# Optimization experiments

Measured on AMD Instinct MI355X. Metric: run time of the kernel, lower is better.

Reference implementation:

```python
import jax, jax.numpy as jnp
import numpy as np

B, SQ, SKV, D, H = 2, 2048, 2048, 1024, 16
HD = D // H

def setup_inputs() -> dict:
    key = jax.random.key(0)
    ks = jax.random.split(key, 11)
    def xavier(k, shape):
        fan_in, fan_out = shape[1], shape[0]
        lim = jnp.sqrt(6.0 / (fan_in + fan_out))
        return jax.random.uniform(k, shape, jnp.float32, -lim, lim)
    return {
        'query': jax.random.normal(ks[0], (B, SQ, D), jnp.float32),
        'key': jax.random.normal(ks[1], (B, SKV, D), jnp.float32),
        'value': jax.random.normal(ks[2], (B, SKV, D), jnp.float32),
        'Wq': xavier(ks[3], (D, D)), 'bq': jnp.zeros((D,), jnp.float32),
        'Wk': xavier(ks[4], (D, D)), 'bk': jnp.zeros((D,), jnp.float32),
        'Wv': xavier(ks[5], (D, D)), 'bv': jnp.zeros((D,), jnp.float32),
        'Wo': xavier(ks[6], (D, D)), 'bo': jnp.zeros((D,), jnp.float32),
    }

def reference(query, key, value, Wq, bq, Wk, bk, Wv, bv, Wo, bo):
    # Linear uses y = x @ W.T + b (torch convention, W: [out, in])
    Q = query @ Wq.T + bq   # [B, SQ, D]
    K = key @ Wk.T + bk     # [B, SKV, D]
    V = value @ Wv.T + bv   # [B, SKV, D]
    Q = Q.reshape(B, SQ, H, HD).transpose(0, 2, 1, 3)   # [B,H,SQ,HD]
    K = K.reshape(B, SKV, H, HD).transpose(0, 2, 1, 3)  # [B,H,SKV,HD]
    V = V.reshape(B, SKV, H, HD).transpose(0, 2, 1, 3)
    scores = jnp.einsum('bhqd,bhkd->bhqk', Q, K) / jnp.sqrt(jnp.float32(HD))
    probs = jax.nn.softmax(scores, axis=-1)  # dropout is identity at eval
    ctx = jnp.einsum('bhqk,bhkd->bhqd', probs, V)
    ctx = ctx.transpose(0, 2, 1, 3).reshape(B, SQ, D)
    return ctx @ Wo.T + bo
```

## Files before the change

### kernel.cpp

```cpp
#include <hip/hip_runtime.h>

#define DIM   1024
#define NHEAD 16
#define HDIM  64
#define BATCH 2
#define SEQ   2048
#define MTOT  4096

typedef unsigned short u16;
typedef unsigned int   u32;
typedef __attribute__((ext_vector_type(8))) short bf16x8;
typedef __attribute__((ext_vector_type(4))) float f32x4;
typedef __attribute__((ext_vector_type(4))) u32   u32x4;

#define QSCALE 0.18033688011112042f
#define EXP2F(x) __builtin_amdgcn_exp2f(x)
#define SWAP32(a, b) asm volatile("v_permlane32_swap_b32 %0, %1" : "+v"(a), "+v"(b))
#define SWAP16(a, b) asm volatile("v_permlane16_swap_b32 %0, %1" : "+v"(a), "+v"(b))

__device__ __forceinline__ void gload_lds16(const void* g, void* l) {
  __builtin_amdgcn_global_load_lds((const __attribute__((address_space(1))) void*)g,
                                   (__attribute__((address_space(3))) void*)l, 16, 0, 0);
}

__device__ __forceinline__ u16 f32_to_bf16(float f) {
  union { float f; u32 u; } v; v.f = f;
  u32 r = v.u + 0x7fffu + ((v.u >> 16) & 1u);
  return (u16)(r >> 16);
}

__device__ __forceinline__ u32 pack_bf16(float a, float b) {
  return (u32)f32_to_bf16(a) | ((u32)f32_to_bf16(b) << 16);
}

struct CvtArgs {
  const float* s[7];
  u16*         d[7];
  int          n8[7];
};

__global__ __launch_bounds__(256) void cvt_all(CvtArgs a) {
  const int z = blockIdx.z;
  const float* s = a.s[z];
  u16* d = a.d[z];
  const int n8 = a.n8[z];
  const int stride = gridDim.x * blockDim.x;
  for (int i = blockIdx.x * blockDim.x + threadIdx.x; i < n8; i += stride) {
    float4 x = ((const float4*)s)[2 * i], y = ((const float4*)s)[2 * i + 1];
    u32x4 o;
    o[0] = pack_bf16(x.x, x.y); o[1] = pack_bf16(x.z, x.w);
    o[2] = pack_bf16(y.x, y.y); o[3] = pack_bf16(y.z, y.w);
    *(u32x4*)&d[(size_t)i * 8] = o;
  }
}

template<int MF, bool OUTF32, bool BIAS_ROW>
__device__ __forceinline__ void gemm_body(
    const u16* __restrict__ X, const u16* __restrict__ W,
    const float* __restrict__ bias, void* __restrict__ Cv, int ldc, float scale,
    int m0, int n0)
{
  __shared__ __align__(16) u16 ldsA[32 * 4 * 64];
  __shared__ __align__(16) u16 ldsB[128 * 64];
  const int tid  = threadIdx.x;
  const int lane = tid & 63;
  const int wid  = tid >> 6;
  const int wr   = wid >> 1, wc = wid & 1;
  const int srow = tid >> 3;
  const int scs  = tid & 7;

  f32x4 acc[MF][4];
#pragma unroll
  for (int mf = 0; mf < MF; ++mf)
#pragma unroll
    for (int nf = 0; nf < 4; ++nf)
#pragma unroll
      for (int r = 0; r < 4; ++r) acc[mf][nf][r] = 0.f;

  for (int kt = 0; kt < DIM; kt += 64) {
    __syncthreads();
#pragma unroll
    for (int call = 0; call < MF; ++call) {
      int row = call * 32 + srow;
      int lc  = scs ^ (row & 7);
      gload_lds16(X + (size_t)(m0 + row) * DIM + kt + lc * 8,
                  &ldsA[(row * 8 + scs) * 8]);
    }
#pragma unroll
    for (int call = 0; call < 4; ++call) {
      int row = call * 32 + srow;
      int lc  = scs ^ (row & 7);
      gload_lds16(W + (size_t)(n0 + row) * DIM + kt + lc * 8,
                  &ldsB[(row * 8 + scs) * 8]);
    }
    __syncthreads();
#pragma unroll
    for (int ks = 0; ks < 2; ++ks) {
      bf16x8 af[MF], bfr[4];
#pragma unroll
      for (int mf = 0; mf < MF; ++mf) {
        int row = wr * (16 * MF) + mf * 16 + (lane & 15);
        int ch  = (ks * 4 + (lane >> 4)) ^ (row & 7);
        af[mf] = *(const bf16x8*)&ldsA[row * 64 + ch * 8];
      }
#pragma unroll
      for (int nf = 0; nf < 4; ++nf) {
        int row = wc * 64 + nf * 16 + (lane & 15);
        int ch  = (ks * 4 + (lane >> 4)) ^ (row & 7);
        bfr[nf] = *(const bf16x8*)&ldsB[row * 64 + ch * 8];
      }
#pragma unroll
      for (int mf = 0; mf < MF; ++mf)
#pragma unroll
        for (int nf = 0; nf < 4; ++nf)
          acc[mf][nf] = __builtin_amdgcn_mfma_f32_16x16x32_bf16(
              af[mf], bfr[nf], acc[mf][nf], 0, 0, 0);
    }
  }
#pragma unroll
  for (int nf = 0; nf < 4; ++nf) {
    int col = n0 + wc * 64 + nf * 16 + (lane & 15);
    float bcol = BIAS_ROW ? 0.f : bias[col];
#pragma unroll
    for (int mf = 0; mf < MF; ++mf) {
      int rbase = m0 + wr * (16 * MF) + mf * 16 + ((lane >> 4) << 2);
#pragma unroll
      for (int r = 0; r < 4; ++r) {
        float bv = BIAS_ROW ? bias[rbase + r] : bcol;
        float v = (acc[mf][nf][r] + bv) * scale;
        if (OUTF32) ((float*)Cv)[(size_t)(rbase + r) * ldc + col] = v;
        else        ((u16*)Cv)[(size_t)(rbase + r) * ldc + col] = f32_to_bf16(v);
      }
    }
  }
}

__global__ __launch_bounds__(256, 2) void gemm_proj_kernel(
    const u16* __restrict__ q, const u16* __restrict__ k, const u16* __restrict__ v,
    const u16* __restrict__ wq, const u16* __restrict__ wk, const u16* __restrict__ wv,
    const float* __restrict__ bq, const float* __restrict__ bk, const float* __restrict__ bv,
    u16* __restrict__ oq, u16* __restrict__ ok, u16* __restrict__ ovt)
{
  const int bid = blockIdx.x;
  const int wk_ = (bid & 7) * 96 + (bid >> 3);
  const int z = wk_ >> 8, rem = wk_ & 255;
  const int ty = rem >> 3, tx = rem & 7;
  if (z == 0)
    gemm_body<4, false, false>(q, wq, bq, oq, DIM, QSCALE, ty * 128, tx * 128);
  else if (z == 1)
    gemm_body<4, false, false>(k, wk, bk, ok, DIM, 1.0f, ty * 128, tx * 128);
  else
    gemm_body<4, false, true>(wv, v, bv, ovt, MTOT, 1.0f, tx * 128, ty * 128);
}

__global__ __launch_bounds__(256, 2) void gemm_o_kernel(
    const u16* __restrict__ x, const u16* __restrict__ w,
    const float* __restrict__ b, float* __restrict__ c)
{
  const int bid = blockIdx.x;
  const int wk_ = (bid & 7) * 64 + (bid >> 3);
  const int ty = wk_ >> 3, tx = wk_ & 7;
  gemm_body<2, true, false>(x, w, b, c, DIM, 1.0f, ty * 64, tx * 128);
}

__global__ __launch_bounds__(256, 2) void attn_kernel(
    const u16* __restrict__ Qm, const u16* __restrict__ Km,
    const u16* __restrict__ Vt, u16* __restrict__ Cm)
{
  __shared__ __align__(16) u16 Kl[2][128 * 64];
  __shared__ __align__(16) u16 Vl[2][64 * 128];

  const int tid = threadIdx.x, lane = tid & 63, wid = tid >> 6;
  const int c = lane & 15, g = lane >> 4;
  const int wkid = (blockIdx.x & 7) * 64 + (blockIdx.x >> 3);
  const int qt = wkid & 15;
  const int bh = wkid >> 4;
  const int b = bh >> 4, h = bh & 15;
  const size_t hb = (size_t)h * HDIM;
  const int q0 = qt * 128 + wid * 32;
  const u16* Qh = Qm + ((size_t)b * SEQ + q0) * DIM + hb;
  const u16* Kh = Km + (size_t)b * SEQ * DIM + hb;
  const u16* Vh = Vt + (size_t)(h * HDIM) * MTOT + (size_t)b * SEQ;

  bf16x8 qf[2][2];
#pragma unroll
  for (int mf = 0; mf < 2; ++mf)
#pragma unroll
    for (int ks = 0; ks < 2; ++ks)
      qf[mf][ks] = *(const bf16x8*)(Qh + (size_t)(16 * mf + c) * DIM + ks * 32 + g * 8);

  bf16x8 ones;
#pragma unroll
  for (int j = 0; j < 8; ++j) ((short*)&ones)[j] = (short)0x3F80;

  f32x4 oacc[2][4], lacc[2];
#pragma unroll
  for (int mf = 0; mf < 2; ++mf) {
#pragma unroll
    for (int nd = 0; nd < 4; ++nd)
#pragma unroll
      for (int r = 0; r < 4; ++r) oacc[mf][nd][r] = 0.f;
#pragma unroll
    for (int r = 0; r < 4; ++r) lacc[mf][r] = 0.f;
  }

  const int srow = tid >> 3, scs = tid & 7;
  const int srow2 = tid >> 4, scs2 = tid & 15;

#define STAGE(T, BUF)                                                          \
  {                                                                            \
    const int kvs = (T) * 128;                                                 \
    _Pragma("unroll")                                                          \
    for (int call = 0; call < 4; ++call) {                                     \
      int row = call * 32 + srow;                                              \
      int lc  = scs ^ (row & 7);                                               \
      gload_lds16(Kh + (size_t)(kvs + row) * DIM + lc * 8,                     \
                  &Kl[BUF][(row * 8 + scs) * 8]);                              \
    }                                                                          \
    _Pragma("unroll")                                                          \
    for (int call = 0; call < 4; ++call) {                                     \
      int row = call * 16 + srow2;                                             \
      int lc  = scs2 ^ (row & 15);                                             \
      gload_lds16(Vh + (size_t)row * MTOT + kvs + lc * 8,                      \
                  &Vl[BUF][(row * 16 + scs2) * 8]);                            \
    }                                                                          \
  }

  STAGE(0, 0);

  for (int t = 0; t < 16; ++t) {
    const int cur = t & 1;
    if (t < 15) {
      STAGE(t + 1, cur ^ 1);
      asm volatile("s_waitcnt vmcnt(8)" ::: "memory");
    } else {
      asm volatile("s_waitcnt vmcnt(0)" ::: "memory");
    }
    __builtin_amdgcn_sched_barrier(0);
    __builtin_amdgcn_s_barrier();
    __builtin_amdgcn_sched_barrier(0);
    __builtin_amdgcn_s_setprio(1);

    u32 W[8][2][2];
#pragma unroll
    for (int nvk = 0; nvk < 8; ++nvk) {
      int row = nvk * 16 + c;
      f32x4 sacc[2];
#pragma unroll
      for (int mf = 0; mf < 2; ++mf)
#pragma unroll
        for (int r = 0; r < 4; ++r) sacc[mf][r] = 0.f;
#pragma unroll
      for (int ks = 0; ks < 2; ++ks) {
        int ch = (ks * 4 + g) ^ (row & 7);
        bf16x8 kf = *(const bf16x8*)&Kl[cur][row * 64 + ch * 8];
#pragma unroll
        for (int mf = 0; mf < 2; ++mf)
          sacc[mf] = __builtin_amdgcn_mfma_f32_16x16x32_bf16(
              kf, qf[mf][ks], sacc[mf], 0, 0, 0);
      }
#pragma unroll
      for (int mf = 0; mf < 2; ++mf) {
        W[nvk][mf][0] = pack_bf16(EXP2F(sacc[mf][0]), EXP2F(sacc[mf][1]));
        W[nvk][mf][1] = pack_bf16(EXP2F(sacc[mf][2]), EXP2F(sacc[mf][3]));
      }
    }

#pragma unroll
    for (int ks = 0; ks < 4; ++ks) {
      bf16x8 vfr[4];
#pragma unroll
      for (int nd = 0; nd < 4; ++nd) {
        int row = nd * 16 + c;
        int ch  = (ks * 4 + g) ^ (row & 15);
        vfr[nd] = *(const bf16x8*)&Vl[cur][row * 128 + ch * 8];
      }
#pragma unroll
      for (int mf = 0; mf < 2; ++mf) {
        u32 a0 = W[2 * ks][mf][0], b0 = W[2 * ks + 1][mf][0];
        u32 a1 = W[2 * ks][mf][1], b1 = W[2 * ks + 1][mf][1];
        SWAP32(a0, b0); SWAP16(a0, b0);
        SWAP32(a1, b1); SWAP16(a1, b1);
        u32x4 pw4; pw4[0] = a0; pw4[1] = a1; pw4[2] = b0; pw4[3] = b1;
        bf16x8 pa = __builtin_bit_cast(bf16x8, pw4);
        lacc[mf] = __builtin_amdgcn_mfma_f32_16x16x32_bf16(
            pa, ones, lacc[mf], 0, 0, 0);
#pragma unroll
        for (int nd = 0; nd < 4; ++nd)
          oacc[mf][nd] = __builtin_amdgcn_mfma_f32_16x16x32_bf16(
              pa, vfr[nd], oacc[mf][nd], 0, 0, 0);
      }
    }

    __builtin_amdgcn_s_setprio(0);
    __builtin_amdgcn_sched_barrier(0);
    __builtin_amdgcn_s_barrier();
  }
#undef STAGE

#pragma unroll
  for (int mf = 0; mf < 2; ++mf)
#pragma unroll
    for (int nd = 0; nd < 4; ++nd)
#pragma unroll
      for (int r = 0; r < 4; ++r) {
        int q = q0 + 16 * mf + 4 * g + r;
        float v = oacc[mf][nd][r] / lacc[mf][r];
        Cm[((size_t)b * SEQ + q) * DIM + hb + nd * 16 + c] = f32_to_bf16(v);
      }
}

extern "C" void kernel_launch(void* const* d_in, const int* in_sizes, int n_in,
                              void* d_out, int out_size, void* d_ws, size_t ws_size,
                              hipStream_t stream)
{
  const float* query = (const float*)d_in[0];
  const float* key   = (const float*)d_in[1];
  const float* value = (const float*)d_in[2];
  const float* Wq = (const float*)d_in[3];  const float* bq = (const float*)d_in[4];
  const float* Wk = (const float*)d_in[5];  const float* bk = (const float*)d_in[6];
  const float* Wv = (const float*)d_in[7];  const float* bv = (const float*)d_in[8];
  const float* Wo = (const float*)d_in[9];  const float* bo = (const float*)d_in[10];
  float* out = (float*)d_out;

  const size_t NQKV = (size_t)MTOT * DIM;
  const size_t NW   = (size_t)DIM * DIM;
  u16* base = (u16*)d_ws;
  u16* Qb  = base;
  u16* Kb  = Qb + NQKV;
  u16* Vtb = Kb + NQKV;
  u16* Cb  = Vtb + NQKV;
  u16* qc  = Cb + NQKV;
  u16* kc  = qc + NQKV;
  u16* vc  = kc + NQKV;
  u16* wqc = vc + NQKV;
  u16* wkc = wqc + NW;
  u16* wvc = wkc + NW;
  u16* woc = wvc + NW;

  CvtArgs ca;
  ca.s[0] = query; ca.s[1] = key; ca.s[2] = value;
  ca.s[3] = Wq; ca.s[4] = Wk; ca.s[5] = Wv; ca.s[6] = Wo;
  ca.d[0] = qc; ca.d[1] = kc; ca.d[2] = vc;
  ca.d[3] = wqc; ca.d[4] = wkc; ca.d[5] = wvc; ca.d[6] = woc;
  for (int i = 0; i < 3; ++i) ca.n8[i] = (int)(NQKV / 8);
  for (int i = 3; i < 7; ++i) ca.n8[i] = (int)(NW / 8);
  cvt_all<<<dim3(256, 1, 7), 256, 0, stream>>>(ca);

  dim3 blk(256);
  gemm_proj_kernel<<<768, blk, 0, stream>>>(
      qc, kc, vc, wqc, wkc, wvc, bq, bk, bv, Qb, Kb, Vtb);
  attn_kernel<<<512, blk, 0, stream>>>(Qb, Kb, Vtb, Cb);
  gemm_o_kernel<<<512, blk, 0, stream>>>(Cb, woc, bo, out);
}
```

Baseline: 120.9 us.

## Double-buffer GEMM LDS tiles to overlap global loads with MFMA compute

Splits the GEMM shared-memory tiles into two buffers and prefetches the next K-tile with global_load_lds while the current tile is consumed by MFMAs. Explicit vmcnt waits and s_barriers replace the two __syncthreads per iteration, so load latency can hide behind compute. This doubles LDS use per block, which may lower occupancy, and it relies on hand-counted vmcnt values being correct for each MF.

Measured after the change: 141.0 us. +16.6%, slower.

```diff
diff --git a/kernel.cpp b/kernel.cpp
--- a/kernel.cpp
+++ b/kernel.cpp
@@ -60,8 +60,8 @@
     const float* __restrict__ bias, void* __restrict__ Cv, int ldc, float scale,
     int m0, int n0)
 {
-  __shared__ __align__(16) u16 ldsA[32 * 4 * 64];
-  __shared__ __align__(16) u16 ldsB[128 * 64];
+  __shared__ __align__(16) u16 ldsA[2][MF * 32 * 64];
+  __shared__ __align__(16) u16 ldsB[2][128 * 64];
   const int tid  = threadIdx.x;
   const int lane = tid & 63;
   const int wid  = tid >> 6;
@@ -77,23 +77,40 @@
 #pragma unroll
       for (int r = 0; r < 4; ++r) acc[mf][nf][r] = 0.f;
 
-  for (int kt = 0; kt < DIM; kt += 64) {
-    __syncthreads();
-#pragma unroll
-    for (int call = 0; call < MF; ++call) {
-      int row = call * 32 + srow;
-      int lc  = scs ^ (row & 7);
-      gload_lds16(X + (size_t)(m0 + row) * DIM + kt + lc * 8,
-                  &ldsA[(row * 8 + scs) * 8]);
-    }
-#pragma unroll
-    for (int call = 0; call < 4; ++call) {
-      int row = call * 32 + srow;
-      int lc  = scs ^ (row & 7);
-      gload_lds16(W + (size_t)(n0 + row) * DIM + kt + lc * 8,
-                  &ldsB[(row * 8 + scs) * 8]);
-    }
-    __syncthreads();
+#define GSTAGE(TI, BUF)                                                        \
+  {                                                                            \
+    const int kt = (TI) * 64;                                                  \
+    _Pragma("unroll")                                                          \
+    for (int call = 0; call < MF; ++call) {                                    \
+      int row = call * 32 + srow;                                              \
+      int lc  = scs ^ (row & 7);                                               \
+      gload_lds16(X + (size_t)(m0 + row) * DIM + kt + lc * 8,                  \
+                  &ldsA[BUF][(row * 8 + scs) * 8]);                            \
+    }                                                                          \
+    _Pragma("unroll")                                                          \
+    for (int call = 0; call < 4; ++call) {                                     \
+      int row = call * 32 + srow;                                              \
+      int lc  = scs ^ (row & 7);                                               \
+      gload_lds16(W + (size_t)(n0 + row) * DIM + kt + lc * 8,                  \
+                  &ldsB[BUF][(row * 8 + scs) * 8]);                            \
+    }                                                                          \
+  }
+
+  GSTAGE(0, 0);
+
+  for (int ti = 0; ti < 16; ++ti) {
+    const int cur = ti & 1;
+    if (ti < 15) {
+      GSTAGE(ti + 1, cur ^ 1);
+      if (MF == 4) asm volatile("s_waitcnt vmcnt(8)" ::: "memory");
+      else         asm volatile("s_waitcnt vmcnt(6)" ::: "memory");
+    } else {
+      asm volatile("s_waitcnt vmcnt(0)" ::: "memory");
+    }
+    __builtin_amdgcn_sched_barrier(0);
+    __builtin_amdgcn_s_barrier();
+    __builtin_amdgcn_sched_barrier(0);
+
 #pragma unroll
     for (int ks = 0; ks < 2; ++ks) {
       bf16x8 af[MF], bfr[4];
@@ -101,13 +118,13 @@
       for (int mf = 0; mf < MF; ++mf) {
         int row = wr * (16 * MF) + mf * 16 + (lane & 15);
         int ch  = (ks * 4 + (lane >> 4)) ^ (row & 7);
-        af[mf] = *(const bf16x8*)&ldsA[row * 64 + ch * 8];
+        af[mf] = *(const bf16x8*)&ldsA[cur][row * 64 + ch * 8];
       }
 #pragma unroll
       for (int nf = 0; nf < 4; ++nf) {
         int row = wc * 64 + nf * 16 + (lane & 15);
         int ch  = (ks * 4 + (lane >> 4)) ^ (row & 7);
-        bfr[nf] = *(const bf16x8*)&ldsB[row * 64 + ch * 8];
+        bfr[nf] = *(const bf16x8*)&ldsB[cur][row * 64 + ch * 8];
       }
 #pragma unroll
       for (int mf = 0; mf < MF; ++mf)
@@ -116,7 +133,12 @@
           acc[mf][nf] = __builtin_amdgcn_mfma_f32_16x16x32_bf16(
               af[mf], bfr[nf], acc[mf][nf], 0, 0, 0);
     }
-  }
+
+    __builtin_amdgcn_sched_barrier(0);
+    __builtin_amdgcn_s_barrier();
+  }
+#undef GSTAGE
+
 #pragma unroll
   for (int nf = 0; nf < 4; ++nf) {
     int col = n0 + wc * 64 + nf * 16 + (lane & 15);
```
